# Kernel optimization log

Hardware: AMD Instinct MI355X
Metric: run time of the kernel (lower is better)

The kernel has to match this reference:

```python
import jax, jax.numpy as jnp
import numpy as np

QK_DIM = 64
ATTN_BETA = 1.0 / QK_DIM ** 0.5  # default beta = 1/sqrt(qk_dim)


def setup_inputs() -> dict:
    key = jax.random.key(0)
    k1, k2, k3, k4 = jax.random.split(key, 4)
    B, K, D = 8, 1024, 768
    H, Z = 12, 64
    M = int(D * 4.0)
    g = jax.random.normal(k1, (B, K, D), dtype=jnp.float32)
    wq = jax.random.normal(k2, (H, Z, D), dtype=jnp.float32) * 0.02
    wk = jax.random.normal(k3, (H, Z, D), dtype=jnp.float32) * 0.02
    w_hn = jax.random.normal(k4, (M, D), dtype=jnp.float32) * (1.0 / np.sqrt(D))
    beta_hn = jnp.ones((1,), dtype=jnp.float32) * 0.01
    return {"g": g, "wq": wq, "wk": wk, "w_hn": w_hn, "beta_hn": beta_hn}


def reference(g, wq, wk, w_hn, beta_hn):
    # Attention energy: q,k = per-head projections; E = -1/beta * sum logsumexp(beta * QK^T)
    q = jnp.einsum('bkd,hzd->bkhz', g, wq)  # [B,K,H,Z]
    k = jnp.einsum('bkd,hzd->bkhz', g, wk)  # [B,K,H,Z]
    A = jnp.einsum('bqhz,bkhz->bhqk', q, k)  # [B,H,Q,K]
    attn_e = -1.0 / ATTN_BETA * jnp.sum(jax.nn.logsumexp(ATTN_BETA * A, axis=-1))
    # Hopfield energy: E = -1/beta_hn * sum logsumexp(beta_hn * g W^T)
    h = beta_hn * jnp.einsum('bkd,md->bkm', g, w_hn)  # [B,K,M]
    hn_e = -1.0 / beta_hn * jnp.sum(jax.nn.logsumexp(h, axis=-1))  # shape (1,)
    return attn_e + hn_e  # shape (1,) matching torch broadcast
```

## Files before the change

### kernel.cpp

```cpp
#include <hip/hip_runtime.h>
#include <hip/hip_bf16.h>
#include <stdint.h>
#include <stddef.h>

typedef float  f32x4  __attribute__((ext_vector_type(4)));
typedef float  f32x16 __attribute__((ext_vector_type(16)));
typedef int    i32x8  __attribute__((ext_vector_type(8)));
typedef unsigned char u8;

#define LOG2E  1.44269504f
#define QSCALE 0.18033688f
#define WSC    16.0f
#define IWSC   0.0625f
#define QSTORE 0.36067376f
#define KSTORE 0.5f
#define SCALE_A_M8 0x77777777
#define SCALE_ONE  0x7F7F7F7F

__device__ __forceinline__ void gld_lds16(const void* gptr, void* lptr) {
    __builtin_amdgcn_global_load_lds(
        (const __attribute__((address_space(1))) unsigned int*)gptr,
        (__attribute__((address_space(3))) unsigned int*)lptr,
        16, 0, 0);
}

__global__ void cast_all(const float* __restrict__ g, const float* __restrict__ wq,
                         const float* __restrict__ wk, const float* __restrict__ whn,
                         u8* __restrict__ g_f8, u8* __restrict__ Wcat,
                         float* __restrict__ sums, float* __restrict__ out) {
    int b = blockIdx.x, t = threadIdx.x;
    if (b < 104) {
        float4 z = {0.f, 0.f, 0.f, 0.f};
        *(float4*)(sums + (b * 256 + t) * 4) = z;
        if (b == 0 && t == 0) out[0] = 0.f;
    }
    const float* src; u8* dst; int off; float sc;
    if (b < 6144)      { src = g;   dst = g_f8;           off = 0;    sc = 1.0f; }
    else if (b < 6720) { src = wq;  dst = Wcat;           off = 6144; sc = WSC;  }
    else if (b < 7296) { src = wk;  dst = Wcat + 589824;  off = 6720; sc = WSC;  }
    else               { src = whn; dst = Wcat + 1179648; off = 7296; sc = WSC;  }
    int i = ((b - off) * 256 + t) * 4;
    float4 v = *(const float4*)(src + i);
    int p = __builtin_amdgcn_cvt_pk_fp8_f32(sc * v.x, sc * v.y, 0, false);
    p     = __builtin_amdgcn_cvt_pk_fp8_f32(sc * v.z, sc * v.w, p, true);
    *(int*)(dst + i) = p;
}

__global__ void gemm_fused(const u8* __restrict__ A, const u8* __restrict__ Bm,
                           u8* __restrict__ qkh, float* __restrict__ rowsum,
                           const float* __restrict__ beta_p) {
    __shared__ __align__(16) u8 As[2][8192];
    __shared__ __align__(16) u8 Bs[2][8192];
    const int t = threadIdx.x;
    const int w = t >> 6, l = t & 63;
    const int wm = (w >> 1) * 64, wn = (w & 1) * 64;
    const int tile_m = blockIdx.x * 128;
    const int tile_n = blockIdx.y * 128;

    f32x16 acc[2][2];
#pragma unroll
    for (int i = 0; i < 2; i++)
#pragma unroll
        for (int j = 0; j < 2; j++)
#pragma unroll
            for (int q = 0; q < 16; q++) acc[i][j][q] = 0.f;

    const u8* gA[2]; const u8* gB[2];
#pragma unroll
    for (int i = 0; i < 2; i++) {
        int sl = i * 256 + t, u = sl >> 3;
        int su = (t & 7) ^ (u & 7);
        int row = 2 * u + (su >> 2), ks = su & 3;
        gA[i] = A  + (size_t)(tile_m + row) * 768 + ks * 16;
        gB[i] = Bm + (size_t)(tile_n + row) * 768 + ks * 16;
    }

    const int ln = l & 31, lh = l >> 5;
    const int sb = (ln & 1) * 4 + lh * 2;
    union F8x32 { uint4 q[2]; i32x8 v; };

#pragma unroll
    for (int i = 0; i < 2; i++) {
        gld_lds16(gA[i], As[0] + (i * 256 + t) * 16);
        gld_lds16(gB[i], Bs[0] + (i * 256 + t) * 16);
    }

#pragma unroll
    for (int kk = 0; kk < 12; kk++) {
        const int p = kk & 1;
        __builtin_amdgcn_s_waitcnt(0);
        __syncthreads();
        if (kk < 11) {
#pragma unroll
            for (int i = 0; i < 2; i++) {
                gld_lds16(gA[i] + (kk + 1) * 64, As[p ^ 1] + (i * 256 + t) * 16);
                gld_lds16(gB[i] + (kk + 1) * 64, Bs[p ^ 1] + (i * 256 + t) * 16);
            }
        }
        i32x8 af[2], bf[2];
#pragma unroll
        for (int mi = 0; mi < 2; mi++) {
            int rA = wm + mi * 32 + ln, uA = rA >> 1, u7 = uA & 7;
            F8x32 x;
            x.q[0] = *(const uint4*)(As[p] + uA * 128 + ((sb)     ^ u7) * 16);
            x.q[1] = *(const uint4*)(As[p] + uA * 128 + ((sb + 1) ^ u7) * 16);
            af[mi] = x.v;
            int rB = wn + mi * 32 + ln, uB = rB >> 1, v7 = uB & 7;
            F8x32 y;
            y.q[0] = *(const uint4*)(Bs[p] + uB * 128 + ((sb)     ^ v7) * 16);
            y.q[1] = *(const uint4*)(Bs[p] + uB * 128 + ((sb + 1) ^ v7) * 16);
            bf[mi] = y.v;
        }
#pragma unroll
        for (int mi = 0; mi < 2; mi++)
#pragma unroll
            for (int nj = 0; nj < 2; nj++)
                acc[mi][nj] = __builtin_amdgcn_mfma_scale_f32_32x32x64_f8f6f4(
                    af[mi], bf[nj], acc[mi][nj], 0, 0, 0, SCALE_ONE, 0, SCALE_ONE);
    }

    if (tile_n < 1536) {
        const int tt = (tile_n >= 768);
        const int bb = tile_m >> 10;
        const int m7 = tile_m & 1023;
        const float sc = tt ? KSTORE : QSTORE;
#pragma unroll
        for (int mi = 0; mi < 2; mi++)
#pragma unroll
            for (int nj = 0; nj < 2; nj++) {
                const int colbase = tile_n - tt * 768 + wn + nj * 32;
                const int hh = colbase >> 6;
                const int z  = (colbase & 63) + ln;
                u8* base = qkh + ((size_t)((bb * 12 + hh) * 2 + tt) << 16);
#pragma unroll
                for (int r = 0; r < 16; r++) {
                    int kr = m7 + wm + mi * 32 + (r & 3) + 8 * (r >> 2) + 4 * lh;
                    int u = kr >> 1, u7 = u & 7;
                    int slot = ((kr & 1) * 4 + (z >> 4)) ^ u7;
                    int pv = __builtin_amdgcn_cvt_pk_fp8_f32(sc * acc[mi][nj][r], 0.f, 0, false);
                    base[(size_t)u * 128 + slot * 16 + (z & 15)] = (u8)(pv & 0xFF);
                }
            }
    } else {
        const float sc2 = beta_p[0] * LOG2E * IWSC;
#pragma unroll
        for (int mi = 0; mi < 2; mi++)
#pragma unroll
            for (int r = 0; r < 16; r++) {
                float s = __builtin_amdgcn_exp2f(sc2 * acc[mi][0][r])
                        + __builtin_amdgcn_exp2f(sc2 * acc[mi][1][r]);
                s += __shfl_xor(s, 1, 32);
                s += __shfl_xor(s, 2, 32);
                s += __shfl_xor(s, 4, 32);
                s += __shfl_xor(s, 8, 32);
                s += __shfl_xor(s, 16, 32);
                if (ln == 0)
                    atomicAdd(&rowsum[tile_m + wm + mi * 32 + (r & 3) + 8 * (r >> 2) + 4 * lh], s);
            }
    }
}

__global__ void __launch_bounds__(256, 4)
attn_energy(const u8* __restrict__ qkh, float* __restrict__ arow) {
    __shared__ __align__(16) u8 Sk[32768];
    const int t = threadIdx.x, w = t >> 6, l = t & 63;
    const int qt = blockIdx.x >> 1, kh = blockIdx.x & 1;
    const int h = blockIdx.y, b = blockIdx.z;
    const u8* qp = qkh + ((size_t)((b * 12 + h) * 2 + 0) << 16) + qt * 8192;
    const u8* kp = qkh + ((size_t)((b * 12 + h) * 2 + 1) << 16) + kh * 32768;

#pragma unroll
    for (int i = 0; i < 8; i++)
        gld_lds16(kp + (i * 256 + t) * 16, Sk + (i * 256 + t) * 16);

    const int ln = l & 31, lh = l >> 5;
    union F8x32 { uint4 q[2]; i32x8 v; };

    const int rA = w * 32 + ln, uA = rA >> 1, u7A = uA & 7;
    const int sA = (rA & 1) * 4 + lh * 2;
    F8x32 ua;
    ua.q[0] = *(const uint4*)(qp + uA * 128 + ((sA)     ^ u7A) * 16);
    ua.q[1] = *(const uint4*)(qp + uA * 128 + ((sA + 1) ^ u7A) * 16);

    float rs[16];
#pragma unroll
    for (int r = 0; r < 16; r++) rs[r] = 0.f;

    __builtin_amdgcn_s_waitcnt(0);
    __syncthreads();

#pragma unroll 2
    for (int nt = 0; nt < 16; nt++) {
        const int rB = nt * 32 + ln, uB = rB >> 1, u7B = uB & 7;
        const int sB = (rB & 1) * 4 + lh * 2;
        F8x32 ub;
        ub.q[0] = *(const uint4*)(Sk + uB * 128 + ((sB)     ^ u7B) * 16);
        ub.q[1] = *(const uint4*)(Sk + uB * 128 + ((sB + 1) ^ u7B) * 16);
        f32x16 acc;
#pragma unroll
        for (int q = 0; q < 16; q++) acc[q] = 0.f;
        acc = __builtin_amdgcn_mfma_scale_f32_32x32x64_f8f6f4(
            ua.v, ub.v, acc, 0, 0, 0, SCALE_A_M8, 0, SCALE_ONE);
#pragma unroll
        for (int r = 0; r < 16; r++) rs[r] += __builtin_amdgcn_exp2f(acc[r]);
    }

    const int rowbase = (b * 12 + h) * 1024 + qt * 128 + w * 32 + lh * 4;
#pragma unroll
    for (int r = 0; r < 16; r++) {
        float v = rs[r];
        v += __shfl_xor(v, 1, 32);
        v += __shfl_xor(v, 2, 32);
        v += __shfl_xor(v, 4, 32);
        v += __shfl_xor(v, 8, 32);
        v += __shfl_xor(v, 16, 32);
        if (ln == 0)
            atomicAdd(&arow[rowbase + (r & 3) + 8 * (r >> 2)], v);
    }
}

__global__ void finalize(const float* __restrict__ sums, const float* __restrict__ beta_p,
                         float* __restrict__ out) {
    __shared__ float wpart[4];
    const int t = threadIdx.x, w = t >> 6, l = t & 63;
    const int i = blockIdx.x * 256 + t;
    float v;
    if (i < 8192) v = (-1.f / beta_p[0]) * __logf(sums[i]);
    else          v = -8.f * __logf(sums[i]);
    for (int o = 32; o > 0; o >>= 1) v += __shfl_down(v, o, 64);
    if (l == 0) wpart[w] = v;
    __syncthreads();
    if (t == 0) atomicAdd(out, wpart[0] + wpart[1] + wpart[2] + wpart[3]);
}

extern "C" void kernel_launch(void* const* d_in, const int* in_sizes, int n_in,
                              void* d_out, int out_size, void* d_ws, size_t ws_size,
                              hipStream_t stream) {
    const float* g    = (const float*)d_in[0];
    const float* wq   = (const float*)d_in[1];
    const float* wk   = (const float*)d_in[2];
    const float* w_hn = (const float*)d_in[3];
    const float* beta = (const float*)d_in[4];
    float* out = (float*)d_out;

    char* ws = (char*)d_ws;
    u8*    g_f8   = (u8*)(ws);
    u8*    Wcat   = (u8*)(ws + 6291456);
    u8*    qkh    = (u8*)(ws + 9830400);
    float* sums   = (float*)(ws + 22413312);
    float* rowsum = sums;
    float* arow   = sums + 8192;

    cast_all<<<9600, 256, 0, stream>>>(g, wq, wk, w_hn, g_f8, Wcat, sums, out);

    dim3 gg(64, 36);
    gemm_fused<<<gg, 256, 0, stream>>>(g_f8, Wcat, qkh, rowsum, beta);

    dim3 ga(16, 12, 8);
    attn_energy<<<ga, 256, 0, stream>>>(qkh, arow);

    finalize<<<416, 256, 0, stream>>>(sums, beta, out);
}
```

Measured before the change: 161.1 us.

## Replace double-buffered 64-wide K pipeline with single-buffered 128-wide K tiles

The GEMM main loop drops its double-buffered LDS prefetch of 64-byte K slices and instead loads a full 128-wide K tile into a single buffer. It then waits, runs two MFMA sub-steps, and synchronizes again before the next load. This halves the number of barrier/wait rounds and uses a simpler row-based swizzle, but global loads no longer overlap with MFMA compute inside a block. Overlap now depends on other resident blocks for occupancy.

Result: faster. 153.0 us (-5.0%).

```diff
diff --git a/kernel.cpp b/kernel.cpp
--- a/kernel.cpp
+++ b/kernel.cpp
@@ -49,8 +49,8 @@
 __global__ void gemm_fused(const u8* __restrict__ A, const u8* __restrict__ Bm,
                            u8* __restrict__ qkh, float* __restrict__ rowsum,
                            const float* __restrict__ beta_p) {
-    __shared__ __align__(16) u8 As[2][8192];
-    __shared__ __align__(16) u8 Bs[2][8192];
+    __shared__ __align__(16) u8 As[128 * 128];
+    __shared__ __align__(16) u8 Bs[128 * 128];
     const int t = threadIdx.x;
     const int w = t >> 6, l = t & 63;
     const int wm = (w >> 1) * 64, wn = (w & 1) * 64;
@@ -65,58 +65,48 @@
 #pragma unroll
             for (int q = 0; q < 16; q++) acc[i][j][q] = 0.f;
 
-    const u8* gA[2]; const u8* gB[2];
-#pragma unroll
-    for (int i = 0; i < 2; i++) {
-        int sl = i * 256 + t, u = sl >> 3;
-        int su = (t & 7) ^ (u & 7);
-        int row = 2 * u + (su >> 2), ks = su & 3;
-        gA[i] = A  + (size_t)(tile_m + row) * 768 + ks * 16;
-        gB[i] = Bm + (size_t)(tile_n + row) * 768 + ks * 16;
-    }
+    const int srow = t >> 3;
+    const int sswz = (t & 7) ^ (srow & 7);
+    const u8* gA = A  + (size_t)(tile_m + srow) * 768 + sswz * 16;
+    const u8* gB = Bm + (size_t)(tile_n + srow) * 768 + sswz * 16;
 
     const int ln = l & 31, lh = l >> 5;
-    const int sb = (ln & 1) * 4 + lh * 2;
     union F8x32 { uint4 q[2]; i32x8 v; };
 
-#pragma unroll
-    for (int i = 0; i < 2; i++) {
-        gld_lds16(gA[i], As[0] + (i * 256 + t) * 16);
-        gld_lds16(gB[i], Bs[0] + (i * 256 + t) * 16);
-    }
-
-#pragma unroll
-    for (int kk = 0; kk < 12; kk++) {
-        const int p = kk & 1;
+    for (int k0 = 0; k0 < 768; k0 += 128) {
+#pragma unroll
+        for (int i = 0; i < 4; i++) {
+            gld_lds16(gA + (size_t)i * 32 * 768 + k0, As + (i * 256 + t) * 16);
+            gld_lds16(gB + (size_t)i * 32 * 768 + k0, Bs + (i * 256 + t) * 16);
+        }
         __builtin_amdgcn_s_waitcnt(0);
         __syncthreads();
-        if (kk < 11) {
-#pragma unroll
-            for (int i = 0; i < 2; i++) {
-                gld_lds16(gA[i] + (kk + 1) * 64, As[p ^ 1] + (i * 256 + t) * 16);
-                gld_lds16(gB[i] + (kk + 1) * 64, Bs[p ^ 1] + (i * 256 + t) * 16);
+
+#pragma unroll
+        for (int ks = 0; ks < 2; ks++) {
+            const int s = ks * 4 + lh * 2;
+            i32x8 af[2], bf[2];
+#pragma unroll
+            for (int mi = 0; mi < 2; mi++) {
+                int rA = wm + mi * 32 + ln, r7 = rA & 7;
+                F8x32 x;
+                x.q[0] = *(const uint4*)(As + rA * 128 + ((s)     ^ r7) * 16);
+                x.q[1] = *(const uint4*)(As + rA * 128 + ((s + 1) ^ r7) * 16);
+                af[mi] = x.v;
+                int rB = wn + mi * 32 + ln, b7 = rB & 7;
+                F8x32 y;
+                y.q[0] = *(const uint4*)(Bs + rB * 128 + ((s)     ^ b7) * 16);
+                y.q[1] = *(const uint4*)(Bs + rB * 128 + ((s + 1) ^ b7) * 16);
+                bf[mi] = y.v;
             }
+#pragma unroll
+            for (int mi = 0; mi < 2; mi++)
+#pragma unroll
+                for (int nj = 0; nj < 2; nj++)
+                    acc[mi][nj] = __builtin_amdgcn_mfma_scale_f32_32x32x64_f8f6f4(
+                        af[mi], bf[nj], acc[mi][nj], 0, 0, 0, SCALE_ONE, 0, SCALE_ONE);
         }
-        i32x8 af[2], bf[2];
-#pragma unroll
-        for (int mi = 0; mi < 2; mi++) {
-            int rA = wm + mi * 32 + ln, uA = rA >> 1, u7 = uA & 7;
-            F8x32 x;
-            x.q[0] = *(const uint4*)(As[p] + uA * 128 + ((sb)     ^ u7) * 16);
-            x.q[1] = *(const uint4*)(As[p] + uA * 128 + ((sb + 1) ^ u7) * 16);
-            af[mi] = x.v;
-            int rB = wn + mi * 32 + ln, uB = rB >> 1, v7 = uB & 7;
-            F8x32 y;
-            y.q[0] = *(const uint4*)(Bs[p] + uB * 128 + ((sb)     ^ v7) * 16);
-            y.q[1] = *(const uint4*)(Bs[p] + uB * 128 + ((sb + 1) ^ v7) * 16);
-            bf[mi] = y.v;
-        }
-#pragma unroll
-        for (int mi = 0; mi < 2; mi++)
-#pragma unroll
-            for (int nj = 0; nj < 2; nj++)
-                acc[mi][nj] = __builtin_amdgcn_mfma_scale_f32_32x32x64_f8f6f4(
-                    af[mi], bf[nj], acc[mi][nj], 0, 0, 0, SCALE_ONE, 0, SCALE_ONE);
+        __syncthreads();
     }
 
     if (tile_n < 1536) {
```
